# Optimization experiments

Measured on AMD Instinct MI355X. Metric: run time of the kernel, lower is better.

## Reference

```python
import jax, jax.numpy as jnp
import numpy as np

EPS = 1e-5  # torch BatchNorm default eps


def _bn_relu(x, g, b, relu):
    # Training-mode BatchNorm1d over (N, C, L): stats over axes (0, 2).
    m = jnp.mean(x, axis=(0, 2), keepdims=True)
    v = jnp.var(x, axis=(0, 2), keepdims=True)
    y = (x - m) * jax.lax.rsqrt(v + EPS) * g[None, :, None] + b[None, :, None]
    return jax.nn.relu(y) if relu else y


def setup_inputs() -> dict:
    key = jax.random.key(0)
    k0, k1, k2 = jax.random.split(key, 3)
    N, C, H = 256, 512, 64  # batch, channels (inplanes==planes), spatial positions (mask_channel)
    x = jax.random.normal(k0, (N, C, H), dtype=jnp.float32)
    # LocallyConnected2d weights: torch shape (1, out, in, H, 1, k^2=1) -> (out, in, H)
    w1 = jax.random.normal(k1, (C, C, H), dtype=jnp.float32) * 0.02
    w2 = jax.random.normal(k2, (C, C, H), dtype=jnp.float32) * 0.02
    g1 = jnp.ones((C,), jnp.float32)
    b1 = jnp.zeros((C,), jnp.float32)
    g2 = jnp.ones((C,), jnp.float32)
    b2 = jnp.zeros((C,), jnp.float32)
    return {"x": x, "w1": w1, "g1": g1, "b1": b1, "w2": w2, "g2": g2, "b2": b2}


def reference(x, w1, g1, b1, w2, g2, b2):
    # conv1: locally-connected 1x1 -> per-position matmul over channels
    out = jnp.einsum('nch,och->noh', x, w1)          # (N, C, H)
    out = _bn_relu(out, g1, b1, relu=True)
    # conv2
    out = jnp.einsum('nch,och->noh', out, w2)
    out = _bn_relu(out, g2, b2, relu=False)
    # residual add (downsample is None) + final relu
    return jax.nn.relu(out + x)
```

## Files before the change

kernel.cpp:

```cpp
#include <hip/hip_runtime.h>
#include <stdint.h>

typedef float  f32x4  __attribute__((ext_vector_type(4)));
typedef __bf16 bf16x8 __attribute__((ext_vector_type(8)));
typedef __bf16 bf16x4 __attribute__((ext_vector_type(4)));

#define N_ 256
#define C_ 512
#define H_ 64
#define RS_ 32768

__device__ __forceinline__ uint32_t pack_bf16x2(float a, float b) {
  const uint16_t ua = __builtin_bit_cast(uint16_t, (__bf16)a);
  const uint16_t ub = __builtin_bit_cast(uint16_t, (__bf16)b);
  return (uint32_t)ua | ((uint32_t)ub << 16);
}

__global__ __launch_bounds__(256) void k_prep_all(const float* __restrict__ x,
                                                  const float* __restrict__ w1,
                                                  const float* __restrict__ w2,
                                                  __bf16* __restrict__ xT,
                                                  __bf16* __restrict__ w1T,
                                                  __bf16* __restrict__ w2T,
                                                  float* __restrict__ stats) {
  __shared__ uint32_t lds[4][64 * 33];
  const int t = threadIdx.x, wid = t >> 6, l = t & 63;
  if (blockIdx.x == 0) {
#pragma unroll
    for (int i = 0; i < 8; ++i) stats[i * 256 + t] = 0.f;
  }
  uint32_t* my = lds[wid];
  const int gw = blockIdx.x * 4 + wid;

  for (int task = gw; task < 10240; task += 2560) {
    const float* src;
    __bf16* dst;
    int u;
    if (task < 2048)      { src = x;  dst = xT;  u = task; }
    else if (task < 6144) { src = w1; dst = w1T; u = task - 2048; }
    else                  { src = w2; dst = w2T; u = task - 6144; }
    const int p = u >> 3, cb = u & 7;
    const float* sb = src + ((size_t)p * 512 + cb * 64) * 64;

#pragma unroll
    for (int i = 0; i < 16; ++i) {
      const int c  = i * 4 + (l >> 4);
      const int hq = l & 15;
      const float4 v = *reinterpret_cast<const float4*>(sb + c * 64 + hq * 4);
      my[c * 33 + 2 * hq]     = pack_bf16x2(v.x, v.y);
      my[c * 33 + 2 * hq + 1] = pack_bf16x2(v.z, v.w);
    }

    __bf16* db = dst + (size_t)p * RS_ + cb * 64;
#pragma unroll
    for (int s = 0; s < 8; ++s) {
      const int h  = s * 8 + (l >> 3);
      const int a  = l & 7;
      const int hm = h >> 1;
      const bool odd = (h & 1) != 0;
      uint32_t W[8];
#pragma unroll
      for (int i = 0; i < 8; ++i) W[i] = my[(a * 8 + i) * 33 + hm];
      uint4 o;
      uint32_t* op = reinterpret_cast<uint32_t*>(&o);
#pragma unroll
      for (int k = 0; k < 4; ++k) {
        const uint32_t wa = W[2 * k], wb = W[2 * k + 1];
        op[k] = odd ? ((wa >> 16) | (wb & 0xFFFF0000u))
                    : ((wa & 0xFFFFu) | (wb << 16));
      }
      *reinterpret_cast<uint4*>(db + (size_t)h * 512 + a * 8) = o;
    }
  }
}

template <bool BN_A>
__device__ __forceinline__ void gemm_body(
    const __bf16* __restrict__ A, const __bf16* __restrict__ B,
    __bf16* __restrict__ Co,
    const float* __restrict__ sum_in, const float* __restrict__ sq_in,
    const float* __restrict__ g, const float* __restrict__ bb,
    float* __restrict__ sum_out, float* __restrict__ sq_out,
    int gblk, int tid, __bf16* AsB, __bf16* BsB,
    float* a_lds, float* c_lds) {
  const int wkid = (gblk & 7) * 64 + (gblk >> 3);
  const int h  = wkid >> 3;
  const int tm = (wkid >> 2) & 1, tn = wkid & 3;
  const int m0 = tm * 128, n0 = tn * 128;
  const __bf16* Ah = A + (size_t)m0 * RS_ + (size_t)h * C_;
  const __bf16* Bh = B + (size_t)n0 * RS_ + (size_t)h * C_;
  const int lane = tid & 63, wid = tid >> 6;
  const int wr = wid >> 1, wc = wid & 1;
  const int lrow8 = lane >> 3;
  const int swz   = (lane & 7) ^ lrow8;

  if (BN_A) {
#pragma unroll
    for (int ch = tid; ch < 512; ch += 256) {
      const float m    = sum_in[ch] * (1.f / 16384.f);
      const float var  = fmaxf(0.f, sq_in[ch] * (1.f / 16384.f) - m * m);
      const float aa   = g[ch] * rsqrtf(var + 1e-5f);
      a_lds[ch] = aa;
      c_lds[ch] = bb[ch] - m * aa;
    }
    __syncthreads();
  }

  auto stage_b = [&](int buf, int kt) {
#pragma unroll
    for (int i = 0; i < 4; ++i) {
      const int rbase = wid * 32 + i * 8;
      const __bf16* gb = Bh + (size_t)(rbase + lrow8) * RS_ + kt * 64 + swz * 8;
      __builtin_amdgcn_global_load_lds(
          (const __attribute__((address_space(1))) void*)gb,
          (__attribute__((address_space(3))) void*)(BsB + buf * 8192 + rbase * 64),
          16, 0, 0);
    }
  };
  auto stage_a = [&](int buf, int kt) {
#pragma unroll
    for (int i = 0; i < 4; ++i) {
      const int rbase = wid * 32 + i * 8;
      const __bf16* ga = Ah + (size_t)(rbase + lrow8) * RS_ + kt * 64 + swz * 8;
      __builtin_amdgcn_global_load_lds(
          (const __attribute__((address_space(1))) void*)ga,
          (__attribute__((address_space(3))) void*)(AsB + buf * 8192 + rbase * 64),
          16, 0, 0);
    }
  };
  const int lr32 = tid >> 3, cch = tid & 7;
  auto load_a = [&](bf16x8* v, int kt) {
#pragma unroll
    for (int i = 0; i < 4; ++i)
      v[i] = *reinterpret_cast<const bf16x8*>(
          Ah + (size_t)(i * 32 + lr32) * RS_ + kt * 64 + cch * 8);
  };
  auto bn_write = [&](const bf16x8* v, int buf, int kt) {
    const int cg = kt * 64 + cch * 8;
    const f32x4 s0 = *reinterpret_cast<const f32x4*>(&a_lds[cg]);
    const f32x4 s1 = *reinterpret_cast<const f32x4*>(&a_lds[cg + 4]);
    const f32x4 h0 = *reinterpret_cast<const f32x4*>(&c_lds[cg]);
    const f32x4 h1 = *reinterpret_cast<const f32x4*>(&c_lds[cg + 4]);
#pragma unroll
    for (int i = 0; i < 4; ++i) {
      const int row = i * 32 + lr32;
      bf16x8 y;
#pragma unroll
      for (int e = 0; e < 4; ++e) {
        y[e]     = (__bf16)fmaxf(0.f, fmaf((float)v[i][e],     s0[e], h0[e]));
        y[e + 4] = (__bf16)fmaxf(0.f, fmaf((float)v[i][e + 4], s1[e], h1[e]));
      }
      const int boff = row * 128 + ((cch * 16) ^ ((row & 7) << 4));
      *reinterpret_cast<bf16x8*>(reinterpret_cast<char*>(AsB + buf * 8192) + boff) = y;
    }
  };

  f32x4 acc[4][4] = {};
  const int fr = lane & 15, kc = lane >> 4;
  auto compute = [&](int buf) {
#pragma unroll
    for (int kk = 0; kk < 2; ++kk) {
      bf16x8 af[4], bfq[4];
#pragma unroll
      for (int mf = 0; mf < 4; ++mf) {
        const int row  = wr * 64 + mf * 16 + fr;
        const int boff = row * 128 + ((kk * 64 + kc * 16) ^ ((row & 7) << 4));
        af[mf] = *reinterpret_cast<const bf16x8*>(
            reinterpret_cast<const char*>(AsB + buf * 8192) + boff);
      }
#pragma unroll
      for (int nf = 0; nf < 4; ++nf) {
        const int row  = wc * 64 + nf * 16 + fr;
        const int boff = row * 128 + ((kk * 64 + kc * 16) ^ ((row & 7) << 4));
        bfq[nf] = *reinterpret_cast<const bf16x8*>(
            reinterpret_cast<const char*>(BsB + buf * 8192) + boff);
      }
#pragma unroll
      for (int mf = 0; mf < 4; ++mf)
#pragma unroll
        for (int nf = 0; nf < 4; ++nf)
          acc[mf][nf] = __builtin_amdgcn_mfma_f32_16x16x32_bf16(af[mf], bfq[nf], acc[mf][nf], 0, 0, 0);
    }
  };

  if (BN_A) {
    bf16x8 v0[4];
    load_a(v0, 0);
    bn_write(v0, 0, 0);
  } else {
    stage_a(0, 0);
  }
  stage_b(0, 0);
  __syncthreads();

  int buf = 0;
  for (int kt = 0; kt < 8; ++kt) {
    bf16x8 vn[4];
    if (kt < 7) {
      stage_b(buf ^ 1, kt + 1);
      if (!BN_A) stage_a(buf ^ 1, kt + 1);
      else       load_a(vn, kt + 1);
    }
    compute(buf);
    if (BN_A && kt < 7) bn_write(vn, buf ^ 1, kt + 1);
    __syncthreads();
    buf ^= 1;
  }

  const int rq = (lane >> 4) * 4;
#pragma unroll
  for (int nf = 0; nf < 4; ++nf) {
    const int oc = n0 + wc * 64 + nf * 16 + fr;
    float s = 0.f, s2 = 0.f;
#pragma unroll
    for (int mf = 0; mf < 4; ++mf) {
      const int rb = m0 + wr * 64 + mf * 16 + rq;
      f32x4 v = acc[mf][nf];
#pragma unroll
      for (int j = 0; j < 4; ++j) {
        const float f = v[j];
        Co[(size_t)(rb + j) * RS_ + (size_t)h * C_ + oc] = (__bf16)f;
        s += f;
        s2 += f * f;
      }
    }
    s  += __shfl_xor(s, 16);  s  += __shfl_xor(s, 32);
    s2 += __shfl_xor(s2, 16); s2 += __shfl_xor(s2, 32);
    if (lane < 16) {
      atomicAdd(&sum_out[oc], s);
      atomicAdd(&sq_out[oc], s2);
    }
  }
}

__global__ __launch_bounds__(256, 2) void k_gemm1(
    const __bf16* __restrict__ xT, const __bf16* __restrict__ w1T,
    __bf16* __restrict__ t1T,
    float* __restrict__ sum1, float* __restrict__ sq1) {
  __shared__ __bf16 As[2][8192];
  __shared__ __bf16 Bs[2][8192];
  gemm_body<false>(xT, w1T, t1T, nullptr, nullptr, nullptr, nullptr,
                   sum1, sq1, (int)blockIdx.x, (int)threadIdx.x,
                   &As[0][0], &Bs[0][0], nullptr, nullptr);
}

__global__ __launch_bounds__(256, 2) void k_gemm2(
    const __bf16* __restrict__ t1T, const __bf16* __restrict__ w2T,
    __bf16* __restrict__ t2T,
    const float* __restrict__ sum1, const float* __restrict__ sq1,
    const float* __restrict__ g1, const float* __restrict__ b1,
    float* __restrict__ sum2, float* __restrict__ sq2) {
  __shared__ __bf16 As[2][8192];
  __shared__ __bf16 Bs[2][8192];
  __shared__ float a_lds[512], c_lds[512];
  gemm_body<true>(t1T, w2T, t2T, sum1, sq1, g1, b1, sum2, sq2,
                  (int)blockIdx.x, (int)threadIdx.x,
                  &As[0][0], &Bs[0][0], a_lds, c_lds);
}

__global__ __launch_bounds__(256) void k_finalize(const __bf16* __restrict__ t2,
                                                  const float* __restrict__ x,
                                                  const float* __restrict__ sum2,
                                                  const float* __restrict__ sq2,
                                                  const float* __restrict__ g2,
                                                  const float* __restrict__ b2,
                                                  float* __restrict__ out) {
  __shared__ float tile[64][65];
  __shared__ float a2s[64], c2s[64];
  const int n  = blockIdx.y;
  const int o0 = blockIdx.x * 64;
  const int t  = threadIdx.x;
  if (t < 64) {
    const int o = o0 + t;
    const float m    = sum2[o] * (1.f / 16384.f);
    const float var  = fmaxf(0.f, sq2[o] * (1.f / 16384.f) - m * m);
    const float a    = g2[o] * rsqrtf(var + 1e-5f);
    a2s[t] = a;
    c2s[t] = b2[o] - m * a;
  }
  const __bf16* tb = t2 + (size_t)n * RS_ + o0;
#pragma unroll
  for (int j = 0; j < 4; ++j) {
    const int hh = j * 16 + (t >> 4);
    const int ol = (t & 15) * 4;
    const bf16x4 v = *reinterpret_cast<const bf16x4*>(tb + (size_t)hh * 512 + ol);
#pragma unroll
    for (int e = 0; e < 4; ++e) tile[hh][ol + e] = (float)v[e];
  }
  __syncthreads();
  const int ol = t >> 2;
  const int hb = (t & 3) * 16;
  const int o  = o0 + ol;
  const float a = a2s[ol], c = c2s[ol];
  const float4* xp = reinterpret_cast<const float4*>(x + ((size_t)n * C_ + o) * H_ + hb);
  float4* op = reinterpret_cast<float4*>(out + ((size_t)n * C_ + o) * H_ + hb);
#pragma unroll
  for (int i4 = 0; i4 < 4; ++i4) {
    const float4 xv = xp[i4];
    float4 r;
    r.x = fmaxf(0.f, fmaf(a, tile[hb + i4 * 4 + 0][ol], c) + xv.x);
    r.y = fmaxf(0.f, fmaf(a, tile[hb + i4 * 4 + 1][ol], c) + xv.y);
    r.z = fmaxf(0.f, fmaf(a, tile[hb + i4 * 4 + 2][ol], c) + xv.z);
    r.w = fmaxf(0.f, fmaf(a, tile[hb + i4 * 4 + 3][ol], c) + xv.w);
    op[i4] = r;
  }
}

extern "C" void kernel_launch(void* const* d_in, const int* in_sizes, int n_in,
                              void* d_out, int out_size, void* d_ws, size_t ws_size,
                              hipStream_t stream) {
  const float* x  = (const float*)d_in[0];
  const float* w1 = (const float*)d_in[1];
  const float* g1 = (const float*)d_in[2];
  const float* b1 = (const float*)d_in[3];
  const float* w2 = (const float*)d_in[4];
  const float* g2 = (const float*)d_in[5];
  const float* b2 = (const float*)d_in[6];
  float* out = (float*)d_out;

  char* ws = (char*)d_ws;
  float* stats = (float*)ws;
  float* sum1 = stats,        *sq1 = stats + 512;
  float* sum2 = stats + 1024, *sq2 = stats + 1536;
  const size_t MB = (size_t)1 << 20;
  __bf16* xT  = (__bf16*)(ws + 64 * 1024);
  __bf16* w1T = (__bf16*)(ws + 64 * 1024 + 16 * MB);
  __bf16* w2T = (__bf16*)(ws + 64 * 1024 + 48 * MB);
  __bf16* t1T = (__bf16*)(ws + 64 * 1024 + 80 * MB);
  __bf16* t2T = (__bf16*)(ws + 64 * 1024 + 96 * MB);

  k_prep_all<<<640, 256, 0, stream>>>(x, w1, w2, xT, w1T, w2T, stats);
  k_gemm1<<<512, 256, 0, stream>>>(xT, w1T, t1T, sum1, sq1);
  k_gemm2<<<512, 256, 0, stream>>>(t1T, w2T, t2T, sum1, sq1, g1, b1, sum2, sq2);
  k_finalize<<<dim3(8, 256), 256, 0, stream>>>(t2T, x, sum2, sq2, g2, b2, out);
}
```

Measured before the change: 120.0 us.

## Transpose whole 512x64 row slab per block with swizzled shared-memory tile

The prep kernel now gives each block one full 512-channel by 64-position slab, instead of having each wavefront loop over 64-channel chunks. The slab is staged in a large shared-memory tile with a rotating swizzle on the column index to avoid bank conflicts on the transposed reads. Each output row is then written as a full contiguous 1 KB row per wavefront. The aim is more parallelism and wider, more coalesced stores. In exchange it uses about 66 KB of shared memory per block, which limits occupancy, and adds a block-wide barrier.

Measured after the change: 109.5 us. -8.7%, faster.

```diff
diff --git a/kernel.cpp b/kernel.cpp
--- a/kernel.cpp
+++ b/kernel.cpp
@@ -23,54 +23,52 @@
                                                   __bf16* __restrict__ w1T,
                                                   __bf16* __restrict__ w2T,
                                                   float* __restrict__ stats) {
-  __shared__ uint32_t lds[4][64 * 33];
-  const int t = threadIdx.x, wid = t >> 6, l = t & 63;
-  if (blockIdx.x == 0) {
+  __shared__ uint32_t tile[512 * 33];
+  const int t  = threadIdx.x;
+  const int wv = t >> 6, l = t & 63;
+  const int bid = blockIdx.x;
+  if (bid == 0) {
 #pragma unroll
     for (int i = 0; i < 8; ++i) stats[i * 256 + t] = 0.f;
   }
-  uint32_t* my = lds[wid];
-  const int gw = blockIdx.x * 4 + wid;
-
-  for (int task = gw; task < 10240; task += 2560) {
-    const float* src;
-    __bf16* dst;
-    int u;
-    if (task < 2048)      { src = x;  dst = xT;  u = task; }
-    else if (task < 6144) { src = w1; dst = w1T; u = task - 2048; }
-    else                  { src = w2; dst = w2T; u = task - 6144; }
-    const int p = u >> 3, cb = u & 7;
-    const float* sb = src + ((size_t)p * 512 + cb * 64) * 64;
-
-#pragma unroll
-    for (int i = 0; i < 16; ++i) {
-      const int c  = i * 4 + (l >> 4);
-      const int hq = l & 15;
-      const float4 v = *reinterpret_cast<const float4*>(sb + c * 64 + hq * 4);
-      my[c * 33 + 2 * hq]     = pack_bf16x2(v.x, v.y);
-      my[c * 33 + 2 * hq + 1] = pack_bf16x2(v.z, v.w);
-    }
-
-    __bf16* db = dst + (size_t)p * RS_ + cb * 64;
-#pragma unroll
-    for (int s = 0; s < 8; ++s) {
-      const int h  = s * 8 + (l >> 3);
-      const int a  = l & 7;
-      const int hm = h >> 1;
-      const bool odd = (h & 1) != 0;
-      uint32_t W[8];
-#pragma unroll
-      for (int i = 0; i < 8; ++i) W[i] = my[(a * 8 + i) * 33 + hm];
-      uint4 o;
-      uint32_t* op = reinterpret_cast<uint32_t*>(&o);
-#pragma unroll
-      for (int k = 0; k < 4; ++k) {
-        const uint32_t wa = W[2 * k], wb = W[2 * k + 1];
-        op[k] = odd ? ((wa >> 16) | (wb & 0xFFFF0000u))
-                    : ((wa & 0xFFFFu) | (wb << 16));
-      }
-      *reinterpret_cast<uint4*>(db + (size_t)h * 512 + a * 8) = o;
-    }
+  const float* src;
+  __bf16* dst;
+  int p;
+  if (bid < 256)      { src = x;  dst = xT;  p = bid; }
+  else if (bid < 768) { src = w1; dst = w1T; p = bid - 256; }
+  else                { src = w2; dst = w2T; p = bid - 768; }
+  const float* sb = src + (size_t)p * 32768;
+
+#pragma unroll
+  for (int j = 0; j < 32; ++j) {
+    const int idx = j * 256 + t;
+    const int c = idx >> 4, hq = idx & 15;
+    const float4 v = *reinterpret_cast<const float4*>(sb + c * 64 + hq * 4);
+    const int r = c >> 3;
+    tile[c * 33 + ((2 * hq + r) & 31)]     = pack_bf16x2(v.x, v.y);
+    tile[c * 33 + ((2 * hq + 1 + r) & 31)] = pack_bf16x2(v.z, v.w);
+  }
+  __syncthreads();
+
+  __bf16* db = dst + (size_t)p * RS_;
+#pragma unroll
+  for (int rr = 0; rr < 16; ++rr) {
+    const int h  = wv * 16 + rr;
+    const int hm = h >> 1;
+    const bool odd = (h & 1) != 0;
+    uint32_t W[8];
+#pragma unroll
+    for (int i = 0; i < 8; ++i)
+      W[i] = tile[(l * 8 + i) * 33 + ((hm + l) & 31)];
+    uint4 o;
+    uint32_t* op = reinterpret_cast<uint32_t*>(&o);
+#pragma unroll
+    for (int k = 0; k < 4; ++k) {
+      const uint32_t wa = W[2 * k], wb = W[2 * k + 1];
+      op[k] = odd ? ((wa >> 16) | (wb & 0xFFFF0000u))
+                  : ((wa & 0xFFFFu) | (wb << 16));
+    }
+    *reinterpret_cast<uint4*>(db + (size_t)h * 512 + l * 8) = o;
   }
 }
 
@@ -329,7 +327,7 @@
   __bf16* t1T = (__bf16*)(ws + 64 * 1024 + 80 * MB);
   __bf16* t2T = (__bf16*)(ws + 64 * 1024 + 96 * MB);
 
-  k_prep_all<<<640, 256, 0, stream>>>(x, w1, w2, xT, w1T, w2T, stats);
+  k_prep_all<<<1280, 256, 0, stream>>>(x, w1, w2, xT, w1T, w2T, stats);
   k_gemm1<<<512, 256, 0, stream>>>(xT, w1T, t1T, sum1, sq1);
   k_gemm2<<<512, 256, 0, stream>>>(t1T, w2T, t2T, sum1, sq1, g1, b1, sum2, sq2);
   k_finalize<<<dim3(8, 256), 256, 0, stream>>>(t2T, x, sum2, sq2, g2, b2, out);
```

## Restructure prep transpose into fine-grained sweep with nontemporal weight loads

Applied to the files above, without the earlier changes.

The fp32-to-bf16 transpose/prep kernel is reorganized so each wave handles a small 8-channel by 64-position tile, and ten tasks are unrolled per wave across a grid of 2048 blocks instead of 640 blocks with a strided task loop. Weight reads use nontemporal loads so the weights do not displace x in cache, since x is reused later by the finalize stage. The aim is more memory-level parallelism and better occupancy in a bandwidth-bound conversion. In exchange, each store now writes only 16 bytes per row, scattered with a 1KB stride, which may reduce write coalescing.

Measured after the change: 152.2 us. +26.9%, slower.

```diff
diff --git a/kernel.cpp b/kernel.cpp
--- a/kernel.cpp
+++ b/kernel.cpp
@@ -16,61 +16,61 @@
   return (uint32_t)ua | ((uint32_t)ub << 16);
 }
 
-__global__ __launch_bounds__(256) void k_prep_all(const float* __restrict__ x,
-                                                  const float* __restrict__ w1,
-                                                  const float* __restrict__ w2,
-                                                  __bf16* __restrict__ xT,
-                                                  __bf16* __restrict__ w1T,
-                                                  __bf16* __restrict__ w2T,
-                                                  float* __restrict__ stats) {
-  __shared__ uint32_t lds[4][64 * 33];
-  const int t = threadIdx.x, wid = t >> 6, l = t & 63;
+__global__ __launch_bounds__(256) void k_prep_sweep(
+    const float* __restrict__ x, const float* __restrict__ w1,
+    const float* __restrict__ w2,
+    __bf16* __restrict__ xT, __bf16* __restrict__ w1T,
+    __bf16* __restrict__ w2T, float* __restrict__ stats) {
+  __shared__ uint32_t lds[4][264];
+  const int t = threadIdx.x, wv = t >> 6, l = t & 63;
   if (blockIdx.x == 0) {
 #pragma unroll
     for (int i = 0; i < 8; ++i) stats[i * 256 + t] = 0.f;
   }
-  uint32_t* my = lds[wid];
-  const int gw = blockIdx.x * 4 + wid;
-
-  for (int task = gw; task < 10240; task += 2560) {
+  uint32_t* my = lds[wv];
+  const int wgid = blockIdx.x * 4 + wv;
+  const int r0 = l >> 4, w0 = (l & 15) * 2;
+  const int hm = l >> 1;
+  const bool odd = (l & 1) != 0;
+
+#pragma unroll
+  for (int it = 0; it < 10; ++it) {
+    const int g = it * 8192 + wgid;
+    const int p = g >> 6, e = g & 63;
     const float* src;
     __bf16* dst;
-    int u;
-    if (task < 2048)      { src = x;  dst = xT;  u = task; }
-    else if (task < 6144) { src = w1; dst = w1T; u = task - 2048; }
-    else                  { src = w2; dst = w2T; u = task - 6144; }
-    const int p = u >> 3, cb = u & 7;
-    const float* sb = src + ((size_t)p * 512 + cb * 64) * 64;
-
-#pragma unroll
-    for (int i = 0; i < 16; ++i) {
-      const int c  = i * 4 + (l >> 4);
-      const int hq = l & 15;
-      const float4 v = *reinterpret_cast<const float4*>(sb + c * 64 + hq * 4);
-      my[c * 33 + 2 * hq]     = pack_bf16x2(v.x, v.y);
-      my[c * 33 + 2 * hq + 1] = pack_bf16x2(v.z, v.w);
-    }
-
-    __bf16* db = dst + (size_t)p * RS_ + cb * 64;
-#pragma unroll
-    for (int s = 0; s < 8; ++s) {
-      const int h  = s * 8 + (l >> 3);
-      const int a  = l & 7;
-      const int hm = h >> 1;
-      const bool odd = (h & 1) != 0;
-      uint32_t W[8];
-#pragma unroll
-      for (int i = 0; i < 8; ++i) W[i] = my[(a * 8 + i) * 33 + hm];
-      uint4 o;
-      uint32_t* op = reinterpret_cast<uint32_t*>(&o);
-#pragma unroll
-      for (int k = 0; k < 4; ++k) {
-        const uint32_t wa = W[2 * k], wb = W[2 * k + 1];
-        op[k] = odd ? ((wa >> 16) | (wb & 0xFFFF0000u))
-                    : ((wa & 0xFFFFu) | (wb << 16));
-      }
-      *reinterpret_cast<uint4*>(db + (size_t)h * 512 + a * 8) = o;
-    }
+    int pp;
+    bool isx;
+    if (p < 256)      { src = x;  dst = xT;  pp = p;       isx = true;  }
+    else if (p < 768) { src = w1; dst = w1T; pp = p - 256; isx = false; }
+    else              { src = w2; dst = w2T; pp = p - 768; isx = false; }
+    const float* S = src + (size_t)pp * 32768 + e * 512;
+
+    f32x4 v0, v1;
+    if (isx) {
+      v0 = *reinterpret_cast<const f32x4*>(S + l * 4);
+      v1 = *reinterpret_cast<const f32x4*>(S + 256 + l * 4);
+    } else {
+      v0 = __builtin_nontemporal_load(reinterpret_cast<const f32x4*>(S + l * 4));
+      v1 = __builtin_nontemporal_load(reinterpret_cast<const f32x4*>(S + 256 + l * 4));
+    }
+    my[r0 * 33 + w0]           = pack_bf16x2(v0[0], v0[1]);
+    my[r0 * 33 + w0 + 1]       = pack_bf16x2(v0[2], v0[3]);
+    my[(r0 + 4) * 33 + w0]     = pack_bf16x2(v1[0], v1[1]);
+    my[(r0 + 4) * 33 + w0 + 1] = pack_bf16x2(v1[2], v1[3]);
+
+    uint32_t W[8];
+#pragma unroll
+    for (int i = 0; i < 8; ++i) W[i] = my[i * 33 + hm];
+    uint4 o;
+    uint32_t* op = reinterpret_cast<uint32_t*>(&o);
+#pragma unroll
+    for (int k = 0; k < 4; ++k) {
+      const uint32_t wa = W[2 * k], wb = W[2 * k + 1];
+      op[k] = odd ? ((wa >> 16) | (wb & 0xFFFF0000u))
+                  : ((wa & 0xFFFFu) | (wb << 16));
+    }
+    *reinterpret_cast<uint4*>(dst + (size_t)pp * RS_ + (size_t)l * 512 + e * 8) = o;
   }
 }
 
@@ -329,7 +329,7 @@
   __bf16* t1T = (__bf16*)(ws + 64 * 1024 + 80 * MB);
   __bf16* t2T = (__bf16*)(ws + 64 * 1024 + 96 * MB);
 
-  k_prep_all<<<640, 256, 0, stream>>>(x, w1, w2, xT, w1T, w2T, stats);
+  k_prep_sweep<<<2048, 256, 0, stream>>>(x, w1, w2, xT, w1T, w2T, stats);
   k_gemm1<<<512, 256, 0, stream>>>(xT, w1T, t1T, sum1, sq1);
   k_gemm2<<<512, 256, 0, stream>>>(t1T, w2T, t2T, sum1, sq1, g1, b1, sum2, sq2);
   k_finalize<<<dim3(8, 256), 256, 0, stream>>>(t2T, x, sum2, sq2, g2, b2, out);
```
